# Kernel optimization log

Measured on AMD Instinct MI355X. Metric: run time of the kernel, lower is better.

Reference implementation:

```python
import jax, jax.numpy as jnp
import numpy as np

T, H, I, E, K = 1024, 1024, 1024, 16, 4
ALPHA, LIMIT, EPS = 1.702, 7.0, 1e-5


def setup_inputs() -> dict:
    key = jax.random.key(0)
    ks = jax.random.split(key, 8)
    return {
        "x": jax.random.normal(ks[0], (T, H), jnp.float32),
        "norm_w": jnp.ones((H,), jnp.float32) + 0.01 * jax.random.normal(ks[1], (H,), jnp.float32),
        "router_w": 0.02 * jax.random.normal(ks[2], (E, H), jnp.float32),
        "router_b": jnp.zeros((E,), jnp.float32),
        "w13": 0.02 * jax.random.normal(ks[3], (E, H, 2 * I), jnp.float32),
        "b13": 0.01 * jax.random.normal(ks[4], (E, 2 * I), jnp.float32),
        "w2": 0.02 * jax.random.normal(ks[5], (E, I, H), jnp.float32),
        "b2": 0.01 * jax.random.normal(ks[6], (E, H), jnp.float32),
        "manual_weights": jnp.zeros((1, E), jnp.float32),  # zeros => override branch inactive, as in __init__
        "layer_idx": 0,
    }


def _override(g, lw):
    # torch: log_softmax, then force pos-masked experts to max+0.01, neg-masked to min-0.01
    gl = jax.nn.log_softmax(g, axis=-1)
    mx = jnp.max(gl, axis=-1, keepdims=True)
    mn = jnp.min(gl, axis=-1, keepdims=True)
    gl = jnp.where((lw > 0)[None, :], mx + 0.01, gl)
    gl = jnp.where((lw < 0)[None, :], mn - 0.01, gl)
    return gl


def reference(x, norm_w, router_w, router_b, w13, b13, w2, b2, manual_weights, layer_idx):
    # RMSNorm (eps=1e-5)
    t = x * jax.lax.rsqrt(jnp.mean(x * x, axis=-1, keepdims=True) + EPS) * norm_w
    # router logits [T, E]
    g = t @ router_w.T + router_b
    # conditional manual logit override
    lw = manual_weights[layer_idx]
    g = jax.lax.cond(jnp.max(jnp.abs(lw)) > 0,
                     lambda gg: _override(gg, lw),
                     lambda gg: gg, g)
    # top-k routing, renormalize=True (softmax -> topk -> renorm)
    probs = jax.nn.softmax(g, axis=-1)
    topw, topi = jax.lax.top_k(probs, K)
    topw = topw / jnp.sum(topw, axis=-1, keepdims=True)
    # dense combine matrix [T, E] (sparse dispatch in the fused kernel)
    combine = jnp.zeros(g.shape, x.dtype).at[jnp.arange(g.shape[0])[:, None], topi].add(topw)
    # expert compute: gate_up GEMM + swigluoai + down GEMM (dense over experts for the reference)
    h = jnp.einsum('th,ehf->tef', t, w13) + b13          # [T, E, 2I]
    gate = jnp.minimum(h[..., :I], LIMIT)                # clamp(max=limit)
    up = jnp.clip(h[..., I:], -LIMIT, LIMIT)             # clamp(-limit, limit)
    act = (up + 1.0) * gate * jax.nn.sigmoid(ALPHA * gate)
    y = jnp.einsum('tei,eih->teh', act, w2) + b2         # [T, E, H]
    moe = jnp.einsum('te,teh->th', combine, y)           # weighted scatter-combine
    return x + moe
```

## Files before the change

### kernel.cpp

```cpp
#include <hip/hip_runtime.h>

#define T_    1024
#define H_    1024
#define IDIM  1024
#define E_    16
#define TOPK  4
#define ALPHA 1.702f
#define LIMIT 7.0f

typedef __bf16 bf16;
typedef __bf16 bf16x4 __attribute__((ext_vector_type(4)));
typedef __bf16 bf16x8 __attribute__((ext_vector_type(8)));
typedef float  f32x4  __attribute__((ext_vector_type(4)));

#define BARRIER() do { \
    asm volatile("s_waitcnt lgkmcnt(0)" ::: "memory"); \
    __builtin_amdgcn_s_barrier(); } while (0)

__global__ __launch_bounds__(256) void k_rms_router(
    const float* __restrict__ x, const float* __restrict__ nw,
    const float* __restrict__ rw, const float* __restrict__ rb,
    const float* __restrict__ mw, const int* __restrict__ lidx,
    bf16* __restrict__ tB, float* __restrict__ out,
    int* __restrict__ cnt, int* __restrict__ tok_list,
    float* __restrict__ wgt_list)
{
    const int t = blockIdx.x, tid = threadIdx.x;
    const int lane = tid & 63, wave = tid >> 6;
    __shared__ float tbuf[H_];
    __shared__ float red[4];
    __shared__ float logits[E_];

    float4 xv = ((const float4*)(x + (size_t)t * H_))[tid];
    float4 wv = ((const float4*)nw)[tid];
    float ssq = xv.x*xv.x + xv.y*xv.y + xv.z*xv.z + xv.w*xv.w;
    #pragma unroll
    for (int off = 32; off; off >>= 1) ssq += __shfl_xor(ssq, off);
    if (lane == 0) red[wave] = ssq;
    __syncthreads();
    const float rms = rsqrtf((red[0] + red[1] + red[2] + red[3]) * (1.0f / H_) + 1e-5f);

    float4 tv;
    tv.x = xv.x * rms * wv.x;
    tv.y = xv.y * rms * wv.y;
    tv.z = xv.z * rms * wv.z;
    tv.w = xv.w * rms * wv.w;

    ((float4*)(out + (size_t)t * H_))[tid] = xv;
    ((float4*)tbuf)[tid] = tv;
    bf16x4 tb = { (bf16)tv.x, (bf16)tv.y, (bf16)tv.z, (bf16)tv.w };
    *(bf16x4*)(tB + (size_t)t * H_ + tid * 4) = tb;
    __syncthreads();

    #pragma unroll
    for (int ei = 0; ei < 4; ++ei) {
        const int e = wave * 4 + ei;
        const float* wr = rw + (size_t)e * H_;
        float s = 0.f;
        #pragma unroll
        for (int j = 0; j < 16; ++j) {
            const int c = lane + j * 64;
            s += tbuf[c] * wr[c];
        }
        #pragma unroll
        for (int off = 32; off; off >>= 1) s += __shfl_xor(s, off);
        if (lane == 0) logits[e] = s + rb[e];
    }
    __syncthreads();

    if (tid == 0) {
        float g[E_];
        #pragma unroll
        for (int e = 0; e < E_; ++e) g[e] = logits[e];

        const int li = lidx[0];
        float ma = 0.f, lw[E_];
        #pragma unroll
        for (int e = 0; e < E_; ++e) { lw[e] = mw[li * E_ + e]; ma = fmaxf(ma, fabsf(lw[e])); }
        if (ma > 0.f) {
            float mx = -1e30f;
            for (int e = 0; e < E_; ++e) mx = fmaxf(mx, g[e]);
            float se = 0.f;
            for (int e = 0; e < E_; ++e) se += expf(g[e] - mx);
            const float lse = logf(se) + mx;
            float gl[E_], gmx = -1e30f, gmn = 1e30f;
            for (int e = 0; e < E_; ++e) { gl[e] = g[e] - lse; gmx = fmaxf(gmx, gl[e]); gmn = fminf(gmn, gl[e]); }
            for (int e = 0; e < E_; ++e) {
                if (lw[e] > 0.f)      gl[e] = gmx + 0.01f;
                else if (lw[e] < 0.f) gl[e] = gmn - 0.01f;
                g[e] = gl[e];
            }
        }

        float mx = -1e30f;
        #pragma unroll
        for (int e = 0; e < E_; ++e) mx = fmaxf(mx, g[e]);
        float p[E_];
        #pragma unroll
        for (int e = 0; e < E_; ++e) p[e] = expf(g[e] - mx);

        bool used[E_] = {};
        int   idx[TOPK];
        float twv[TOPK];
        float ssum = 0.f;
        for (int k = 0; k < TOPK; ++k) {
            int best = -1; float bv = -1e30f;
            for (int e = 0; e < E_; ++e)
                if (!used[e] && p[e] > bv) { bv = p[e]; best = e; }
            used[best] = true; idx[k] = best; twv[k] = bv; ssum += bv;
        }
        const float inv = 1.f / ssum;
        for (int k = 0; k < TOPK; ++k) {
            const int e = idx[k];
            const int slot = atomicAdd(&cnt[e], 1);
            tok_list[e * T_ + slot] = t;
            wgt_list[e * T_ + slot] = twv[k] * inv;
        }
    }
}

__global__ void k_scan(const int* __restrict__ cnt, int* __restrict__ base,
                       int* __restrict__ tiln, int* __restrict__ tile_e,
                       int* __restrict__ tile_m0)
{
    const int lane = threadIdx.x;
    int c = (lane < E_) ? cnt[lane] : 0;

    int s = c;
    #pragma unroll
    for (int off = 1; off < 16; off <<= 1) {
        int tv = __shfl_up(s, off);
        if ((lane & 15) >= off) s += tv;
    }
    if (lane < E_) base[lane] = s - c;
    if (lane == E_ - 1) base[E_] = s;

    int nt = (lane < E_) ? ((c + 63) >> 6) : 0;
    int ts = nt;
    #pragma unroll
    for (int off = 1; off < 16; off <<= 1) {
        int tv = __shfl_up(ts, off);
        if ((lane & 15) >= off) ts += tv;
    }
    if (lane == E_ - 1) tiln[0] = ts;
    if (lane < E_) {
        const int t0 = ts - nt;
        for (int i = 0; i < nt; ++i) {
            if (t0 + i < 96) { tile_e[t0 + i] = lane; tile_m0[t0 + i] = i * 64; }
        }
    }
}

__global__ __launch_bounds__(256) void k_repack(
    const float* __restrict__ W, bf16* __restrict__ out, int Ndim)
{
    __shared__ float tile[32][260];
    const int e = blockIdx.z, kb = blockIdx.y, n0 = blockIdx.x * 256;
    const int t = threadIdx.x;
    const int nbs = Ndim >> 4;

    const float* src = W + ((size_t)e * 1024 + (size_t)kb * 32) * Ndim + n0;
    #pragma unroll
    for (int i = 0; i < 8; ++i) {
        const int idx = i * 256 + t;
        const int k = idx >> 6, c4 = (idx & 63) * 4;
        float4 v = *(const float4*)(src + (size_t)k * Ndim + c4);
        *(float4*)&tile[k][c4] = v;
    }
    __syncthreads();

    const int f = t >> 4;
    const int lg = (t & 15) * 4;
    bf16* dst = out + (((size_t)(e * nbs + n0 / 16 + f)) * 32 + kb) * 512;
    #pragma unroll
    for (int li = 0; li < 4; ++li) {
        const int l = lg + li, q = l >> 4, r = l & 15;
        bf16x8 p;
        #pragma unroll
        for (int j = 0; j < 8; ++j) p[j] = (bf16)tile[q * 8 + j][f * 16 + r];
        *(bf16x8*)(dst + l * 8) = p;
    }
}

__global__ __launch_bounds__(256) void k_gateup3(
    const bf16* __restrict__ tB, const bf16* __restrict__ w13p,
    const float* __restrict__ b13, const int* __restrict__ cnt,
    const int* __restrict__ base, const int* __restrict__ tiln,
    const int* __restrict__ tile_e, const int* __restrict__ tile_m0,
    const int* __restrict__ tok_list, bf16* __restrict__ act)
{
    const int ti = blockIdx.y;
    if (ti >= tiln[0]) return;
    const int e  = tile_e[ti];
    const int m0 = tile_m0[ti];
    const int ne = cnt[e];

    const int tid = threadIdx.x, lane = tid & 63, wave = tid >> 6;
    const int q = lane >> 4, r = lane & 15;

    __shared__ __align__(16) bf16 As[8 * 64 * 8];

    const int m   = tid >> 2, kq = tid & 3;
    const int mf_s = m >> 4, r_s = m & 15;
    const int kc_s = kq >> 1, q_s = (kq & 1) * 2;
    bf16* wr0 = As + ((size_t)((mf_s * 2 + kc_s) * 64 + q_s * 16 + r_s)) * 8;
    bf16* wr1 = wr0 + 16 * 8;
    int srow = m0 + m; srow = srow < ne ? srow : ne - 1;
    const bf16* pA = tB + (size_t)tok_list[e * T_ + srow] * H_ + kq * 16;

    const int nb_g = blockIdx.x * 4 + wave;
    const bf16* pBg0 = w13p + ((size_t)(e * 128 + nb_g     ) * 32) * 512 + lane * 8;
    const bf16* pBu0 = w13p + ((size_t)(e * 128 + nb_g + 64) * 32) * 512 + lane * 8;

    f32x4 accg[4] = {};
    f32x4 accu[4] = {};
    uint4 ar0a, ar0b, ar1a, ar1b;
    bf16x8 bg0[2], bu0[2], bg1[2], bu1[2];

#define LOADA(A0, A1) do { \
    A0 = *(const uint4*)pA; A1 = *(const uint4*)(pA + 8); pA += 64; } while (0)
#define STAGEA(A0, A1) do { \
    *(uint4*)wr0 = A0; *(uint4*)wr1 = A1; } while (0)
#define LOADB(BG, BU, s) do { \
    const int ss_ = (s) < 16 ? (s) : 15; \
    BG[0] = *(const bf16x8*)(pBg0 + (size_t)ss_ * 1024); \
    BG[1] = *(const bf16x8*)(pBg0 + (size_t)ss_ * 1024 + 512); \
    BU[0] = *(const bf16x8*)(pBu0 + (size_t)ss_ * 1024); \
    BU[1] = *(const bf16x8*)(pBu0 + (size_t)ss_ * 1024 + 512); } while (0)
#define COMPUTE(BG, BU) do { \
    _Pragma("unroll") \
    for (int kc = 0; kc < 2; ++kc) { \
        bf16x8 afr[4]; \
        _Pragma("unroll") \
        for (int mf = 0; mf < 4; ++mf) \
            afr[mf] = *(const bf16x8*)(As + ((size_t)((mf * 2 + kc) * 64 + lane)) * 8); \
        _Pragma("unroll") \
        for (int mf = 0; mf < 4; ++mf) { \
            accg[mf] = __builtin_amdgcn_mfma_f32_16x16x32_bf16(afr[mf], BG[kc], accg[mf], 0, 0, 0); \
            accu[mf] = __builtin_amdgcn_mfma_f32_16x16x32_bf16(afr[mf], BU[kc], accu[mf], 0, 0, 0); \
        } \
    } } while (0)

    LOADA(ar0a, ar0b);
    LOADB(bg0, bu0, 0);
    LOADB(bg1, bu1, 1);
    #pragma unroll 1
    for (int kb = 0; kb < 16; kb += 2) {
        BARRIER();
        STAGEA(ar0a, ar0b);
        LOADA(ar1a, ar1b);
        BARRIER();
        COMPUTE(bg0, bu0);
        LOADB(bg0, bu0, kb + 2);

        BARRIER();
        STAGEA(ar1a, ar1b);
        LOADA(ar0a, ar0b);
        BARRIER();
        COMPUTE(bg1, bu1);
        LOADB(bg1, bu1, kb + 3);
    }
#undef LOADA
#undef STAGEA
#undef LOADB
#undef COMPUTE

    const int sb = base[e];
    const int cg = nb_g * 16 + r;
    const float bgv = b13[e * 2 * IDIM + cg];
    const float buv = b13[e * 2 * IDIM + IDIM + cg];
    #pragma unroll
    for (int mf = 0; mf < 4; ++mf) {
        #pragma unroll
        for (int rg = 0; rg < 4; ++rg) {
            const int row = mf * 16 + q * 4 + rg;
            if (m0 + row < ne) {
                const float hg = accg[mf][rg] + bgv;
                const float hu = accu[mf][rg] + buv;
                const float gt = fminf(hg, LIMIT);
                const float up = fminf(fmaxf(hu, -LIMIT), LIMIT);
                const float av = (up + 1.0f) * gt / (1.0f + expf(-ALPHA * gt));
                act[(size_t)(sb + m0 + row) * IDIM + cg] = (bf16)av;
            }
        }
    }
}

__global__ __launch_bounds__(256) void k_down3(
    const bf16* __restrict__ act, const bf16* __restrict__ w2p,
    const float* __restrict__ b2, const int* __restrict__ cnt,
    const int* __restrict__ base, const int* __restrict__ tiln,
    const int* __restrict__ tile_e, const int* __restrict__ tile_m0,
    const int* __restrict__ tok_list, const float* __restrict__ wgt_list,
    float* __restrict__ out)
{
    const int ti = blockIdx.y;
    if (ti >= tiln[0]) return;
    const int e  = tile_e[ti];
    const int m0 = tile_m0[ti];
    const int ne = cnt[e];
    const int sb = base[e];

    const int tid = threadIdx.x, lane = tid & 63, wave = tid >> 6;
    const int q = lane >> 4, r = lane & 15;

    __shared__ __align__(16) bf16 As[8 * 64 * 8];

    const int m   = tid >> 2, kq = tid & 3;
    const int mf_s = m >> 4, r_s = m & 15;
    const int kc_s = kq >> 1, q_s = (kq & 1) * 2;
    bf16* wr0 = As + ((size_t)((mf_s * 2 + kc_s) * 64 + q_s * 16 + r_s)) * 8;
    bf16* wr1 = wr0 + 16 * 8;
    int srow = m0 + m; srow = srow < ne ? srow : ne - 1;
    const bf16* pA = act + (size_t)(sb + srow) * IDIM + kq * 16;

    const int nb0 = blockIdx.x * 8 + wave * 2;
    const bf16* pB0b = w2p + ((size_t)(e * 64 + nb0    ) * 32) * 512 + lane * 8;
    const bf16* pB1b = w2p + ((size_t)(e * 64 + nb0 + 1) * 32) * 512 + lane * 8;

    f32x4 acc[4][2] = {};
    uint4 ar0a, ar0b, ar1a, ar1b;
    bf16x8 bA0[2], bB0[2], bA1[2], bB1[2];

#define LOADA(A0, A1) do { \
    A0 = *(const uint4*)pA; A1 = *(const uint4*)(pA + 8); pA += 64; } while (0)
#define STAGEA(A0, A1) do { \
    *(uint4*)wr0 = A0; *(uint4*)wr1 = A1; } while (0)
#define LOADB(B0, B1, s) do { \
    const int ss_ = (s) < 16 ? (s) : 15; \
    B0[0] = *(const bf16x8*)(pB0b + (size_t)ss_ * 1024); \
    B0[1] = *(const bf16x8*)(pB0b + (size_t)ss_ * 1024 + 512); \
    B1[0] = *(const bf16x8*)(pB1b + (size_t)ss_ * 1024); \
    B1[1] = *(const bf16x8*)(pB1b + (size_t)ss_ * 1024 + 512); } while (0)
#define COMPUTE(B0, B1) do { \
    _Pragma("unroll") \
    for (int kc = 0; kc < 2; ++kc) { \
        bf16x8 afr[4]; \
        _Pragma("unroll") \
        for (int mf = 0; mf < 4; ++mf) \
            afr[mf] = *(const bf16x8*)(As + ((size_t)((mf * 2 + kc) * 64 + lane)) * 8); \
        _Pragma("unroll") \
        for (int mf = 0; mf < 4; ++mf) { \
            acc[mf][0] = __builtin_amdgcn_mfma_f32_16x16x32_bf16(afr[mf], B0[kc], acc[mf][0], 0, 0, 0); \
            acc[mf][1] = __builtin_amdgcn_mfma_f32_16x16x32_bf16(afr[mf], B1[kc], acc[mf][1], 0, 0, 0); \
        } \
    } } while (0)

    LOADA(ar0a, ar0b);
    LOADB(bA0, bB0, 0);
    LOADB(bA1, bB1, 1);
    #pragma unroll 1
    for (int kb = 0; kb < 16; kb += 2) {
        BARRIER();
        STAGEA(ar0a, ar0b);
        LOADA(ar1a, ar1b);
        BARRIER();
        COMPUTE(bA0, bB0);
        LOADB(bA0, bB0, kb + 2);

        BARRIER();
        STAGEA(ar1a, ar1b);
        LOADA(ar0a, ar0b);
        BARRIER();
        COMPUTE(bA1, bB1);
        LOADB(bA1, bB1, kb + 3);
    }
#undef LOADA
#undef STAGEA
#undef LOADB
#undef COMPUTE

    #pragma unroll
    for (int nf = 0; nf < 2; ++nf) {
        const int ch = (nb0 + nf) * 16 + r;
        const float bb = b2[e * H_ + ch];
        #pragma unroll
        for (int mf = 0; mf < 4; ++mf) {
            #pragma unroll
            for (int rg = 0; rg < 4; ++rg) {
                const int row = mf * 16 + q * 4 + rg;
                const int s = m0 + row;
                if (s < ne) {
                    const int   tok = tok_list[e * T_ + s];
                    const float w   = wgt_list[e * T_ + s];
                    atomicAdd(&out[(size_t)tok * H_ + ch], w * (acc[mf][nf][rg] + bb));
                }
            }
        }
    }
}

__global__ __launch_bounds__(256) void k_gateup(
    const bf16* __restrict__ tB, const float* __restrict__ w13,
    const float* __restrict__ b13, const int* __restrict__ cnt,
    const int* __restrict__ base, const int* __restrict__ tok_list,
    bf16* __restrict__ act)
{
    const int e  = blockIdx.z;
    const int ne = cnt[e];
    const int m0 = blockIdx.y * 64;
    if (m0 >= ne) return;
    const int n0  = blockIdx.x * 64;
    const int tid = threadIdx.x, lane = tid & 63, wave = tid >> 6;

    __shared__ __align__(16) bf16 As[64][40];
    __shared__ __align__(16) bf16 Bg[64][40];
    __shared__ __align__(16) bf16 Bu[64][40];
    __shared__ int stok[64];

    if (tid < 64) {
        const int s = m0 + tid;
        stok[tid] = (s < ne) ? tok_list[e * T_ + s] : -1;
    }
    __syncthreads();

    const int ar = tid >> 2, ak = (tid & 3) * 8;
    const int atok = stok[ar];
    const int bn = tid & 63, bk = wave * 8;
    const size_t wrow = (size_t)(2 * IDIM);
    const float* wbase = w13 + (size_t)e * H_ * wrow + n0 + bn;

    const int wm = wave >> 1, wn = wave & 1;
    const int q = lane >> 4, r = lane & 15;
    f32x4 accg[2][2] = {};
    f32x4 accu[2][2] = {};

    for (int kb = 0; kb < H_ / 32; ++kb) {
        __syncthreads();
        uint4 av = make_uint4(0u, 0u, 0u, 0u);
        if (atok >= 0)
            av = *(const uint4*)(tB + (size_t)atok * H_ + kb * 32 + ak);
        *(uint4*)&As[ar][ak] = av;
        {
            const float* src = wbase + (size_t)(kb * 32 + bk) * wrow;
            bf16x8 pg, pu;
            #pragma unroll
            for (int j = 0; j < 8; ++j) {
                pg[j] = (bf16)src[(size_t)j * wrow];
                pu[j] = (bf16)src[(size_t)j * wrow + IDIM];
            }
            *(bf16x8*)&Bg[bn][bk] = pg;
            *(bf16x8*)&Bu[bn][bk] = pu;
        }
        __syncthreads();
        bf16x8 a[2], bg[2], bu[2];
        a[0]  = *(const bf16x8*)&As[wm * 32 +      r][q * 8];
        a[1]  = *(const bf16x8*)&As[wm * 32 + 16 + r][q * 8];
        bg[0] = *(const bf16x8*)&Bg[wn * 32 +      r][q * 8];
        bg[1] = *(const bf16x8*)&Bg[wn * 32 + 16 + r][q * 8];
        bu[0] = *(const bf16x8*)&Bu[wn * 32 +      r][q * 8];
        bu[1] = *(const bf16x8*)&Bu[wn * 32 + 16 + r][q * 8];
        #pragma unroll
        for (int im = 0; im < 2; ++im)
            #pragma unroll
            for (int in = 0; in < 2; ++in) {
                accg[im][in] = __builtin_amdgcn_mfma_f32_16x16x32_bf16(a[im], bg[in], accg[im][in], 0, 0, 0);
                accu[im][in] = __builtin_amdgcn_mfma_f32_16x16x32_bf16(a[im], bu[in], accu[im][in], 0, 0, 0);
            }
    }

    const int sb = base[e];
    #pragma unroll
    for (int im = 0; im < 2; ++im)
        #pragma unroll
        for (int in = 0; in < 2; ++in)
            #pragma unroll
            for (int rg = 0; rg < 4; ++rg) {
                const int row = wm * 32 + im * 16 + q * 4 + rg;
                const int col = wn * 32 + in * 16 + r;
                if (m0 + row < ne) {
                    const float hg = accg[im][in][rg] + b13[e * 2 * IDIM + n0 + col];
                    const float hu = accu[im][in][rg] + b13[e * 2 * IDIM + IDIM + n0 + col];
                    const float gt = fminf(hg, LIMIT);
                    const float up = fminf(fmaxf(hu, -LIMIT), LIMIT);
                    const float av = (up + 1.0f) * gt / (1.0f + expf(-ALPHA * gt));
                    act[(size_t)(sb + m0 + row) * IDIM + n0 + col] = (bf16)av;
                }
            }
}

__global__ __launch_bounds__(256) void k_down(
    const bf16* __restrict__ act, const float* __restrict__ w2,
    const float* __restrict__ b2, const int* __restrict__ cnt,
    const int* __restrict__ base, const int* __restrict__ tok_list,
    const float* __restrict__ wgt_list, float* __restrict__ out)
{
    const int e  = blockIdx.z;
    const int ne = cnt[e];
    const int m0 = blockIdx.y * 64;
    if (m0 >= ne) return;
    const int n0  = blockIdx.x * 64;
    const int tid = threadIdx.x, lane = tid & 63, wave = tid >> 6;

    __shared__ __align__(16) bf16 As[64][40];
    __shared__ __align__(16) bf16 Bs[64][40];
    __shared__ int   stok[64];
    __shared__ float swgt[64];

    if (tid < 64) {
        const int s = m0 + tid;
        stok[tid] = (s < ne) ? tok_list[e * T_ + s] : -1;
        swgt[tid] = (s < ne) ? wgt_list[e * T_ + s] : 0.f;
    }
    __syncthreads();

    const int sb = base[e];
    const int ar = tid >> 2, ak = (tid & 3) * 8;
    const bool arow_ok = (m0 + ar) < ne;
    const int bn = tid & 63, bk = wave * 8;
    const float* wbase = w2 + (size_t)e * IDIM * H_ + n0 + bn;

    const int wm = wave >> 1, wn = wave & 1;
    const int q = lane >> 4, r = lane & 15;
    f32x4 acc[2][2] = {};

    for (int kb = 0; kb < IDIM / 32; ++kb) {
        __syncthreads();
        uint4 av = make_uint4(0u, 0u, 0u, 0u);
        if (arow_ok)
            av = *(const uint4*)(act + (size_t)(sb + m0 + ar) * IDIM + kb * 32 + ak);
        *(uint4*)&As[ar][ak] = av;
        {
            const float* src = wbase + (size_t)(kb * 32 + bk) * H_;
            bf16x8 pb;
            #pragma unroll
            for (int j = 0; j < 8; ++j) pb[j] = (bf16)src[(size_t)j * H_];
            *(bf16x8*)&Bs[bn][bk] = pb;
        }
        __syncthreads();
        bf16x8 a[2], b[2];
        a[0] = *(const bf16x8*)&As[wm * 32 +      r][q * 8];
        a[1] = *(const bf16x8*)&As[wm * 32 + 16 + r][q * 8];
        b[0] = *(const bf16x8*)&Bs[wn * 32 +      r][q * 8];
        b[1] = *(const bf16x8*)&Bs[wn * 32 + 16 + r][q * 8];
        #pragma unroll
        for (int im = 0; im < 2; ++im)
            #pragma unroll
            for (int in = 0; in < 2; ++in)
                acc[im][in] = __builtin_amdgcn_mfma_f32_16x16x32_bf16(a[im], b[in], acc[im][in], 0, 0, 0);
    }

    #pragma unroll
    for (int im = 0; im < 2; ++im)
        #pragma unroll
        for (int in = 0; in < 2; ++in)
            #pragma unroll
            for (int rg = 0; rg < 4; ++rg) {
                const int row = wm * 32 + im * 16 + q * 4 + rg;
                const int col = wn * 32 + in * 16 + r;
                if (m0 + row < ne) {
                    const int   tok = stok[row];
                    const float w   = swgt[row];
                    atomicAdd(&out[(size_t)tok * H_ + n0 + col], w * (acc[im][in][rg] + b2[e * H_ + n0 + col]));
                }
            }
}

extern "C" void kernel_launch(void* const* d_in, const int* in_sizes, int n_in,
                              void* d_out, int out_size, void* d_ws, size_t ws_size,
                              hipStream_t stream)
{
    const float* x        = (const float*)d_in[0];
    const float* norm_w   = (const float*)d_in[1];
    const float* router_w = (const float*)d_in[2];
    const float* router_b = (const float*)d_in[3];
    const float* w13      = (const float*)d_in[4];
    const float* b13      = (const float*)d_in[5];
    const float* w2       = (const float*)d_in[6];
    const float* b2       = (const float*)d_in[7];
    const float* manual_w = (const float*)d_in[8];
    const int*   layer_i  = (const int*)d_in[9];
    float* out = (float*)d_out;

    char* ws = (char*)d_ws;
    bf16*  tB   = (bf16*)ws;
    bf16*  act  = (bf16*)(ws + (2ull << 20));
    char*  meta = ws + (10ull << 20);
    int*   cnt      = (int*)meta;
    int*   basep    = (int*)(meta + 64);
    int*   tiln     = (int*)(meta + 256);
    int*   tile_e   = (int*)(meta + 512);
    int*   tile_m0  = (int*)(meta + 1024);
    int*   tok_list = (int*)(meta + (16ull << 10));
    float* wgt_list = (float*)(meta + (16ull << 10) + (64ull << 10));
    bf16*  w13p     = (bf16*)(ws + (12ull << 20));
    bf16*  w2p      = (bf16*)(ws + (76ull << 20));

    const bool fast = ws_size >= (108ull << 20);

    hipMemsetAsync(cnt, 0, E_ * sizeof(int), stream);

    k_rms_router<<<T_, 256, 0, stream>>>(x, norm_w, router_w, router_b,
                                         manual_w, layer_i, tB, out,
                                         cnt, tok_list, wgt_list);
    k_scan<<<1, 64, 0, stream>>>(cnt, basep, tiln, tile_e, tile_m0);

    if (fast) {
        dim3 gr13(2 * IDIM / 256, 32, E_);
        k_repack<<<gr13, 256, 0, stream>>>(w13, w13p, 2 * IDIM);
        dim3 gr2(H_ / 256, 32, E_);
        k_repack<<<gr2, 256, 0, stream>>>(w2, w2p, H_);

        dim3 gg(16, 80);
        k_gateup3<<<gg, 256, 0, stream>>>(tB, w13p, b13, cnt, basep, tiln,
                                          tile_e, tile_m0, tok_list, act);
        dim3 gd(8, 80);
        k_down3<<<gd, 256, 0, stream>>>(act, w2p, b2, cnt, basep, tiln,
                                        tile_e, tile_m0, tok_list, wgt_list, out);
    } else {
        dim3 gg(IDIM / 64, T_ / 64, E_);
        k_gateup<<<gg, 256, 0, stream>>>(tB, w13, b13, cnt, basep, tok_list, act);
        dim3 gd(H_ / 64, T_ / 64, E_);
        k_down<<<gd, 256, 0, stream>>>(act, w2, b2, cnt, basep, tok_list, wgt_list, out);
    }
}
```

Baseline: 401.7 us.

## Fuse weight fp32-to-bf16 conversion into GEMM tiles and inline routing scan

Drops the separate repack kernels that converted all expert weights to packed bf16 each call. The GEMM kernels now load fp32 weight rows directly, convert them in registers and stage them into a padded shared-memory B tile. The single-block scan kernel is also removed, and each block computes its own expert/tile assignment from the counts. The aim is to avoid writing and re-reading a full bf16 weight copy and to cut two launches, at the cost of more LDS traffic, more register pressure and fp32 global reads in the main loop.

```diff
diff --git a/kernel.cpp b/kernel.cpp
--- a/kernel.cpp
+++ b/kernel.cpp
@@ -119,86 +119,44 @@
     }
 }
 
-__global__ void k_scan(const int* __restrict__ cnt, int* __restrict__ base,
-                       int* __restrict__ tiln, int* __restrict__ tile_e,
-                       int* __restrict__ tile_m0)
+__device__ __forceinline__ void inline_scan(const int* __restrict__ cnt,
+                                            int ti, int tid, int* sm)
 {
-    const int lane = threadIdx.x;
-    int c = (lane < E_) ? cnt[lane] : 0;
-
-    int s = c;
-    #pragma unroll
-    for (int off = 1; off < 16; off <<= 1) {
-        int tv = __shfl_up(s, off);
-        if ((lane & 15) >= off) s += tv;
-    }
-    if (lane < E_) base[lane] = s - c;
-    if (lane == E_ - 1) base[E_] = s;
-
-    int nt = (lane < E_) ? ((c + 63) >> 6) : 0;
-    int ts = nt;
-    #pragma unroll
-    for (int off = 1; off < 16; off <<= 1) {
-        int tv = __shfl_up(ts, off);
-        if ((lane & 15) >= off) ts += tv;
-    }
-    if (lane == E_ - 1) tiln[0] = ts;
-    if (lane < E_) {
-        const int t0 = ts - nt;
-        for (int i = 0; i < nt; ++i) {
-            if (t0 + i < 96) { tile_e[t0 + i] = lane; tile_m0[t0 + i] = i * 64; }
-        }
-    }
+    if (tid == 0) {
+        int c0[E_];
+        #pragma unroll
+        for (int e = 0; e < E_; ++e) c0[e] = cnt[e];
+        int s = 0, nt = 0, ee = 0, mm0 = 0, nee = 0, sbb = 0;
+        #pragma unroll
+        for (int e = 0; e < E_; ++e) {
+            const int c = c0[e];
+            const int tcnt = (c + 63) >> 6;
+            if (ti >= nt && ti < nt + tcnt) {
+                ee = e; mm0 = (ti - nt) * 64; nee = c; sbb = s;
+            }
+            s += c; nt += tcnt;
+        }
+        sm[0] = nt; sm[1] = ee; sm[2] = mm0; sm[3] = nee; sm[4] = sbb;
+    }
+    __syncthreads();
 }
 
-__global__ __launch_bounds__(256) void k_repack(
-    const float* __restrict__ W, bf16* __restrict__ out, int Ndim)
-{
-    __shared__ float tile[32][260];
-    const int e = blockIdx.z, kb = blockIdx.y, n0 = blockIdx.x * 256;
-    const int t = threadIdx.x;
-    const int nbs = Ndim >> 4;
-
-    const float* src = W + ((size_t)e * 1024 + (size_t)kb * 32) * Ndim + n0;
-    #pragma unroll
-    for (int i = 0; i < 8; ++i) {
-        const int idx = i * 256 + t;
-        const int k = idx >> 6, c4 = (idx & 63) * 4;
-        float4 v = *(const float4*)(src + (size_t)k * Ndim + c4);
-        *(float4*)&tile[k][c4] = v;
-    }
-    __syncthreads();
-
-    const int f = t >> 4;
-    const int lg = (t & 15) * 4;
-    bf16* dst = out + (((size_t)(e * nbs + n0 / 16 + f)) * 32 + kb) * 512;
-    #pragma unroll
-    for (int li = 0; li < 4; ++li) {
-        const int l = lg + li, q = l >> 4, r = l & 15;
-        bf16x8 p;
-        #pragma unroll
-        for (int j = 0; j < 8; ++j) p[j] = (bf16)tile[q * 8 + j][f * 16 + r];
-        *(bf16x8*)(dst + l * 8) = p;
-    }
-}
-
-__global__ __launch_bounds__(256) void k_gateup3(
-    const bf16* __restrict__ tB, const bf16* __restrict__ w13p,
+__global__ __launch_bounds__(256) void k_gateup7(
+    const bf16* __restrict__ tB, const float* __restrict__ w13,
     const float* __restrict__ b13, const int* __restrict__ cnt,
-    const int* __restrict__ base, const int* __restrict__ tiln,
-    const int* __restrict__ tile_e, const int* __restrict__ tile_m0,
     const int* __restrict__ tok_list, bf16* __restrict__ act)
 {
-    const int ti = blockIdx.y;
-    if (ti >= tiln[0]) return;
-    const int e  = tile_e[ti];
-    const int m0 = tile_m0[ti];
-    const int ne = cnt[e];
-
+    const int ti = blockIdx.y, bx = blockIdx.x;
     const int tid = threadIdx.x, lane = tid & 63, wave = tid >> 6;
     const int q = lane >> 4, r = lane & 15;
 
     __shared__ __align__(16) bf16 As[8 * 64 * 8];
+    __shared__ __align__(16) bf16 Bs[1032 * 8];
+    __shared__ int sm[5];
+
+    inline_scan(cnt, ti, tid, sm);
+    if (ti >= sm[0]) return;
+    const int e = sm[1], m0 = sm[2], ne = sm[3], sb = sm[4];
 
     const int m   = tid >> 2, kq = tid & 3;
     const int mf_s = m >> 4, r_s = m & 15;
@@ -208,64 +166,77 @@
     int srow = m0 + m; srow = srow < ne ? srow : ne - 1;
     const bf16* pA = tB + (size_t)tok_list[e * T_ + srow] * H_ + kq * 16;
 
-    const int nb_g = blockIdx.x * 4 + wave;
-    const bf16* pBg0 = w13p + ((size_t)(e * 128 + nb_g     ) * 32) * 512 + lane * 8;
-    const bf16* pBu0 = w13p + ((size_t)(e * 128 + nb_g + 64) * 32) * 512 + lane * 8;
+    const int c4 = tid & 31, q6 = tid >> 5;
+    const int kcs = q6 >> 2, qs = q6 & 3;
+    const int cc = c4 * 4;
+    const int fB = c4 >> 2, r0 = (c4 & 3) * 4;
+    const int RB = fB * 2 + kcs;
+    bf16* bwr = Bs + ((size_t)(RB * 64 + (RB >> 1) + qs * 16 + r0)) * 8;
+    const int col = (cc < 64) ? (bx * 64 + cc) : (IDIM + bx * 64 + (cc - 64));
+    const float* pB = w13 + (size_t)e * H_ * (2 * IDIM)
+                          + (size_t)(kcs * 32 + qs * 8) * (2 * IDIM) + col;
 
     f32x4 accg[4] = {};
     f32x4 accu[4] = {};
-    uint4 ar0a, ar0b, ar1a, ar1b;
-    bf16x8 bg0[2], bu0[2], bg1[2], bu1[2];
-
-#define LOADA(A0, A1) do { \
-    A0 = *(const uint4*)pA; A1 = *(const uint4*)(pA + 8); pA += 64; } while (0)
-#define STAGEA(A0, A1) do { \
-    *(uint4*)wr0 = A0; *(uint4*)wr1 = A1; } while (0)
-#define LOADB(BG, BU, s) do { \
-    const int ss_ = (s) < 16 ? (s) : 15; \
-    BG[0] = *(const bf16x8*)(pBg0 + (size_t)ss_ * 1024); \
-    BG[1] = *(const bf16x8*)(pBg0 + (size_t)ss_ * 1024 + 512); \
-    BU[0] = *(const bf16x8*)(pBu0 + (size_t)ss_ * 1024); \
-    BU[1] = *(const bf16x8*)(pBu0 + (size_t)ss_ * 1024 + 512); } while (0)
-#define COMPUTE(BG, BU) do { \
+    uint4  a0a, a0b, a1a, a1b;
+    f32x4  br0[8], br1[8];
+
+#define LOADA(A0, A1, s) do { const int ss_ = (s) < 16 ? (s) : 15; \
+    A0 = *(const uint4*)(pA + ss_ * 64); \
+    A1 = *(const uint4*)(pA + ss_ * 64 + 8); } while (0)
+#define LOADB(BR, s) do { const int ss_ = (s) < 16 ? (s) : 15; \
+    _Pragma("unroll") \
+    for (int j = 0; j < 8; ++j) \
+        BR[j] = *(const f32x4*)(pB + (size_t)(ss_ * 64 + j) * (2 * IDIM)); } while (0)
+#define STAGEA(A0, A1) do { *(uint4*)wr0 = A0; *(uint4*)wr1 = A1; } while (0)
+#define STAGEB(BR) do { \
+    _Pragma("unroll") \
+    for (int rr = 0; rr < 4; ++rr) { \
+        bf16x8 p; \
+        _Pragma("unroll") \
+        for (int j = 0; j < 8; ++j) p[j] = (bf16)BR[j][rr]; \
+        *(bf16x8*)(bwr + rr * 8) = p; \
+    } } while (0)
+#define COMPUTE() do { \
     _Pragma("unroll") \
     for (int kc = 0; kc < 2; ++kc) { \
         bf16x8 afr[4]; \
         _Pragma("unroll") \
         for (int mf = 0; mf < 4; ++mf) \
             afr[mf] = *(const bf16x8*)(As + ((size_t)((mf * 2 + kc) * 64 + lane)) * 8); \
+        const int Rg = wave * 2 + kc, Ru = (wave + 4) * 2 + kc; \
+        bf16x8 bg = *(const bf16x8*)(Bs + ((size_t)(Rg * 64 + (Rg >> 1) + lane)) * 8); \
+        bf16x8 bu = *(const bf16x8*)(Bs + ((size_t)(Ru * 64 + (Ru >> 1) + lane)) * 8); \
         _Pragma("unroll") \
         for (int mf = 0; mf < 4; ++mf) { \
-            accg[mf] = __builtin_amdgcn_mfma_f32_16x16x32_bf16(afr[mf], BG[kc], accg[mf], 0, 0, 0); \
-            accu[mf] = __builtin_amdgcn_mfma_f32_16x16x32_bf16(afr[mf], BU[kc], accu[mf], 0, 0, 0); \
+            accg[mf] = __builtin_amdgcn_mfma_f32_16x16x32_bf16(afr[mf], bg, accg[mf], 0, 0, 0); \
+            accu[mf] = __builtin_amdgcn_mfma_f32_16x16x32_bf16(afr[mf], bu, accu[mf], 0, 0, 0); \
         } \
     } } while (0)
 
-    LOADA(ar0a, ar0b);
-    LOADB(bg0, bu0, 0);
-    LOADB(bg1, bu1, 1);
+    LOADA(a0a, a0b, 0);
+    LOADB(br0, 0);
     #pragma unroll 1
     for (int kb = 0; kb < 16; kb += 2) {
         BARRIER();
-        STAGEA(ar0a, ar0b);
-        LOADA(ar1a, ar1b);
-        BARRIER();
-        COMPUTE(bg0, bu0);
-        LOADB(bg0, bu0, kb + 2);
-
-        BARRIER();
-        STAGEA(ar1a, ar1b);
-        LOADA(ar0a, ar0b);
-        BARRIER();
-        COMPUTE(bg1, bu1);
-        LOADB(bg1, bu1, kb + 3);
+        STAGEA(a0a, a0b);  STAGEB(br0);
+        LOADA(a1a, a1b, kb + 1);  LOADB(br1, kb + 1);
+        BARRIER();
+        COMPUTE();
+
+        BARRIER();
+        STAGEA(a1a, a1b);  STAGEB(br1);
+        LOADA(a0a, a0b, kb + 2);  LOADB(br0, kb + 2);
+        BARRIER();
+        COMPUTE();
     }
 #undef LOADA
+#undef LOADB
 #undef STAGEA
-#undef LOADB
+#undef STAGEB
 #undef COMPUTE
 
-    const int sb = base[e];
+    const int nb_g = bx * 4 + wave;
     const int cg = nb_g * 16 + r;
     const float bgv = b13[e * 2 * IDIM + cg];
     const float buv = b13[e * 2 * IDIM + IDIM + cg];
@@ -286,25 +257,23 @@
     }
 }
 
-__global__ __launch_bounds__(256) void k_down3(
-    const bf16* __restrict__ act, const bf16* __restrict__ w2p,
+__global__ __launch_bounds__(256) void k_down7(
+    const bf16* __restrict__ act, const float* __restrict__ w2,
     const float* __restrict__ b2, const int* __restrict__ cnt,
-    const int* __restrict__ base, const int* __restrict__ tiln,
-    const int* __restrict__ tile_e, const int* __restrict__ tile_m0,
     const int* __restrict__ tok_list, const float* __restrict__ wgt_list,
     float* __restrict__ out)
 {
-    const int ti = blockIdx.y;
-    if (ti >= tiln[0]) return;
-    const int e  = tile_e[ti];
-    const int m0 = tile_m0[ti];
-    const int ne = cnt[e];
-    const int sb = base[e];
-
+    const int ti = blockIdx.y, bx = blockIdx.x;
     const int tid = threadIdx.x, lane = tid & 63, wave = tid >> 6;
     const int q = lane >> 4, r = lane & 15;
 
     __shared__ __align__(16) bf16 As[8 * 64 * 8];
+    __shared__ __align__(16) bf16 Bs[1032 * 8];
+    __shared__ int sm[5];
+
+    inline_scan(cnt, ti, tid, sm);
+    if (ti >= sm[0]) return;
+    const int e = sm[1], m0 = sm[2], ne = sm[3], sb = sm[4];
 
     const int m   = tid >> 2, kq = tid & 3;
     const int mf_s = m >> 4, r_s = m & 15;
@@ -314,62 +283,75 @@
     int srow = m0 + m; srow = srow < ne ? srow : ne - 1;
     const bf16* pA = act + (size_t)(sb + srow) * IDIM + kq * 16;
 
-    const int nb0 = blockIdx.x * 8 + wave * 2;
-    const bf16* pB0b = w2p + ((size_t)(e * 64 + nb0    ) * 32) * 512 + lane * 8;
-    const bf16* pB1b = w2p + ((size_t)(e * 64 + nb0 + 1) * 32) * 512 + lane * 8;
+    const int c4 = tid & 31, q6 = tid >> 5;
+    const int kcs = q6 >> 2, qs = q6 & 3;
+    const int cc = c4 * 4;
+    const int fB = c4 >> 2, r0 = (c4 & 3) * 4;
+    const int RB = fB * 2 + kcs;
+    bf16* bwr = Bs + ((size_t)(RB * 64 + (RB >> 1) + qs * 16 + r0)) * 8;
+    const float* pB = w2 + (size_t)e * IDIM * H_
+                         + (size_t)(kcs * 32 + qs * 8) * H_ + bx * 128 + cc;
 
     f32x4 acc[4][2] = {};
-    uint4 ar0a, ar0b, ar1a, ar1b;
-    bf16x8 bA0[2], bB0[2], bA1[2], bB1[2];
-
-#define LOADA(A0, A1) do { \
-    A0 = *(const uint4*)pA; A1 = *(const uint4*)(pA + 8); pA += 64; } while (0)
-#define STAGEA(A0, A1) do { \
-    *(uint4*)wr0 = A0; *(uint4*)wr1 = A1; } while (0)
-#define LOADB(B0, B1, s) do { \
-    const int ss_ = (s) < 16 ? (s) : 15; \
-    B0[0] = *(const bf16x8*)(pB0b + (size_t)ss_ * 1024); \
-    B0[1] = *(const bf16x8*)(pB0b + (size_t)ss_ * 1024 + 512); \
-    B1[0] = *(const bf16x8*)(pB1b + (size_t)ss_ * 1024); \
-    B1[1] = *(const bf16x8*)(pB1b + (size_t)ss_ * 1024 + 512); } while (0)
-#define COMPUTE(B0, B1) do { \
+    uint4  a0a, a0b, a1a, a1b;
+    f32x4  br0[8], br1[8];
+
+#define LOADA(A0, A1, s) do { const int ss_ = (s) < 16 ? (s) : 15; \
+    A0 = *(const uint4*)(pA + ss_ * 64); \
+    A1 = *(const uint4*)(pA + ss_ * 64 + 8); } while (0)
+#define LOADB(BR, s) do { const int ss_ = (s) < 16 ? (s) : 15; \
+    _Pragma("unroll") \
+    for (int j = 0; j < 8; ++j) \
+        BR[j] = *(const f32x4*)(pB + (size_t)(ss_ * 64 + j) * H_); } while (0)
+#define STAGEA(A0, A1) do { *(uint4*)wr0 = A0; *(uint4*)wr1 = A1; } while (0)
+#define STAGEB(BR) do { \
+    _Pragma("unroll") \
+    for (int rr = 0; rr < 4; ++rr) { \
+        bf16x8 p; \
+        _Pragma("unroll") \
+        for (int j = 0; j < 8; ++j) p[j] = (bf16)BR[j][rr]; \
+        *(bf16x8*)(bwr + rr * 8) = p; \
+    } } while (0)
+#define COMPUTE() do { \
     _Pragma("unroll") \
     for (int kc = 0; kc < 2; ++kc) { \
         bf16x8 afr[4]; \
         _Pragma("unroll") \
         for (int mf = 0; mf < 4; ++mf) \
             afr[mf] = *(const bf16x8*)(As + ((size_t)((mf * 2 + kc) * 64 + lane)) * 8); \
+        const int R0 = (wave * 2) * 2 + kc, R1 = (wave * 2 + 1) * 2 + kc; \
+        bf16x8 b0 = *(const bf16x8*)(Bs + ((size_t)(R0 * 64 + (R0 >> 1) + lane)) * 8); \
+        bf16x8 b1 = *(const bf16x8*)(Bs + ((size_t)(R1 * 64 + (R1 >> 1) + lane)) * 8); \
         _Pragma("unroll") \
         for (int mf = 0; mf < 4; ++mf) { \
-            acc[mf][0] = __builtin_amdgcn_mfma_f32_16x16x32_bf16(afr[mf], B0[kc], acc[mf][0], 0, 0, 0); \
-            acc[mf][1] = __builtin_amdgcn_mfma_f32_16x16x32_bf16(afr[mf], B1[kc], acc[mf][1], 0, 0, 0); \
+            acc[mf][0] = __builtin_amdgcn_mfma_f32_16x16x32_bf16(afr[mf], b0, acc[mf][0], 0, 0, 0); \
+            acc[mf][1] = __builtin_amdgcn_mfma_f32_16x16x32_bf16(afr[mf], b1, acc[mf][1], 0, 0, 0); \
         } \
     } } while (0)
 
-    LOADA(ar0a, ar0b);
-    LOADB(bA0, bB0, 0);
-    LOADB(bA1, bB1, 1);
+    LOADA(a0a, a0b, 0);
+    LOADB(br0, 0);
     #pragma unroll 1
     for (int kb = 0; kb < 16; kb += 2) {
         BARRIER();
-        STAGEA(ar0a, ar0b);
-        LOADA(ar1a, ar1b);
-        BARRIER();
-        COMPUTE(bA0, bB0);
-        LOADB(bA0, bB0, kb + 2);
-
-        BARRIER();
-        STAGEA(ar1a, ar1b);
-        LOADA(ar0a, ar0b);
-        BARRIER();
-        COMPUTE(bA1, bB1);
-        LOADB(bA1, bB1, kb + 3);
+        STAGEA(a0a, a0b);  STAGEB(br0);
+        LOADA(a1a, a1b, kb + 1);  LOADB(br1, kb + 1);
+        BARRIER();
+        COMPUTE();
+
+        BARRIER();
+        STAGEA(a1a, a1b);  STAGEB(br1);
+        LOADA(a0a, a0b, kb + 2);  LOADB(br0, kb + 2);
+        BARRIER();
+        COMPUTE();
     }
 #undef LOADA
+#undef LOADB
 #undef STAGEA
-#undef LOADB
+#undef STAGEB
 #undef COMPUTE
 
+    const int nb0 = bx * 8 + wave * 2;
     #pragma unroll
     for (int nf = 0; nf < 2; ++nf) {
         const int ch = (nb0 + nf) * 16 + r;
@@ -388,172 +370,6 @@
             }
         }
     }
-}
-
-__global__ __launch_bounds__(256) void k_gateup(
-    const bf16* __restrict__ tB, const float* __restrict__ w13,
-    const float* __restrict__ b13, const int* __restrict__ cnt,
-    const int* __restrict__ base, const int* __restrict__ tok_list,
-    bf16* __restrict__ act)
-{
-    const int e  = blockIdx.z;
-    const int ne = cnt[e];
-    const int m0 = blockIdx.y * 64;
-    if (m0 >= ne) return;
-    const int n0  = blockIdx.x * 64;
-    const int tid = threadIdx.x, lane = tid & 63, wave = tid >> 6;
-
-    __shared__ __align__(16) bf16 As[64][40];
-    __shared__ __align__(16) bf16 Bg[64][40];
-    __shared__ __align__(16) bf16 Bu[64][40];
-    __shared__ int stok[64];
-
-    if (tid < 64) {
-        const int s = m0 + tid;
-        stok[tid] = (s < ne) ? tok_list[e * T_ + s] : -1;
-    }
-    __syncthreads();
-
-    const int ar = tid >> 2, ak = (tid & 3) * 8;
-    const int atok = stok[ar];
-    const int bn = tid & 63, bk = wave * 8;
-    const size_t wrow = (size_t)(2 * IDIM);
-    const float* wbase = w13 + (size_t)e * H_ * wrow + n0 + bn;
-
-    const int wm = wave >> 1, wn = wave & 1;
-    const int q = lane >> 4, r = lane & 15;
-    f32x4 accg[2][2] = {};
-    f32x4 accu[2][2] = {};
-
-    for (int kb = 0; kb < H_ / 32; ++kb) {
-        __syncthreads();
-        uint4 av = make_uint4(0u, 0u, 0u, 0u);
-        if (atok >= 0)
-            av = *(const uint4*)(tB + (size_t)atok * H_ + kb * 32 + ak);
-        *(uint4*)&As[ar][ak] = av;
-        {
-            const float* src = wbase + (size_t)(kb * 32 + bk) * wrow;
-            bf16x8 pg, pu;
-            #pragma unroll
-            for (int j = 0; j < 8; ++j) {
-                pg[j] = (bf16)src[(size_t)j * wrow];
-                pu[j] = (bf16)src[(size_t)j * wrow + IDIM];
-            }
-            *(bf16x8*)&Bg[bn][bk] = pg;
-            *(bf16x8*)&Bu[bn][bk] = pu;
-        }
-        __syncthreads();
-        bf16x8 a[2], bg[2], bu[2];
-        a[0]  = *(const bf16x8*)&As[wm * 32 +      r][q * 8];
-        a[1]  = *(const bf16x8*)&As[wm * 32 + 16 + r][q * 8];
-        bg[0] = *(const bf16x8*)&Bg[wn * 32 +      r][q * 8];
-        bg[1] = *(const bf16x8*)&Bg[wn * 32 + 16 + r][q * 8];
-        bu[0] = *(const bf16x8*)&Bu[wn * 32 +      r][q * 8];
-        bu[1] = *(const bf16x8*)&Bu[wn * 32 + 16 + r][q * 8];
-        #pragma unroll
-        for (int im = 0; im < 2; ++im)
-            #pragma unroll
-            for (int in = 0; in < 2; ++in) {
-                accg[im][in] = __builtin_amdgcn_mfma_f32_16x16x32_bf16(a[im], bg[in], accg[im][in], 0, 0, 0);
-                accu[im][in] = __builtin_amdgcn_mfma_f32_16x16x32_bf16(a[im], bu[in], accu[im][in], 0, 0, 0);
-            }
-    }
-
-    const int sb = base[e];
-    #pragma unroll
-    for (int im = 0; im < 2; ++im)
-        #pragma unroll
-        for (int in = 0; in < 2; ++in)
-            #pragma unroll
-            for (int rg = 0; rg < 4; ++rg) {
-                const int row = wm * 32 + im * 16 + q * 4 + rg;
-                const int col = wn * 32 + in * 16 + r;
-                if (m0 + row < ne) {
-                    const float hg = accg[im][in][rg] + b13[e * 2 * IDIM + n0 + col];
-                    const float hu = accu[im][in][rg] + b13[e * 2 * IDIM + IDIM + n0 + col];
-                    const float gt = fminf(hg, LIMIT);
-                    const float up = fminf(fmaxf(hu, -LIMIT), LIMIT);
-                    const float av = (up + 1.0f) * gt / (1.0f + expf(-ALPHA * gt));
-                    act[(size_t)(sb + m0 + row) * IDIM + n0 + col] = (bf16)av;
-                }
-            }
-}
-
-__global__ __launch_bounds__(256) void k_down(
-    const bf16* __restrict__ act, const float* __restrict__ w2,
-    const float* __restrict__ b2, const int* __restrict__ cnt,
-    const int* __restrict__ base, const int* __restrict__ tok_list,
-    const float* __restrict__ wgt_list, float* __restrict__ out)
-{
-    const int e  = blockIdx.z;
-    const int ne = cnt[e];
-    const int m0 = blockIdx.y * 64;
-    if (m0 >= ne) return;
-    const int n0  = blockIdx.x * 64;
-    const int tid = threadIdx.x, lane = tid & 63, wave = tid >> 6;
-
-    __shared__ __align__(16) bf16 As[64][40];
-    __shared__ __align__(16) bf16 Bs[64][40];
-    __shared__ int   stok[64];
-    __shared__ float swgt[64];
-
-    if (tid < 64) {
-        const int s = m0 + tid;
-        stok[tid] = (s < ne) ? tok_list[e * T_ + s] : -1;
-        swgt[tid] = (s < ne) ? wgt_list[e * T_ + s] : 0.f;
-    }
-    __syncthreads();
-
-    const int sb = base[e];
-    const int ar = tid >> 2, ak = (tid & 3) * 8;
-    const bool arow_ok = (m0 + ar) < ne;
-    const int bn = tid & 63, bk = wave * 8;
-    const float* wbase = w2 + (size_t)e * IDIM * H_ + n0 + bn;
-
-    const int wm = wave >> 1, wn = wave & 1;
-    const int q = lane >> 4, r = lane & 15;
-    f32x4 acc[2][2] = {};
-
-    for (int kb = 0; kb < IDIM / 32; ++kb) {
-        __syncthreads();
-        uint4 av = make_uint4(0u, 0u, 0u, 0u);
-        if (arow_ok)
-            av = *(const uint4*)(act + (size_t)(sb + m0 + ar) * IDIM + kb * 32 + ak);
-        *(uint4*)&As[ar][ak] = av;
-        {
-            const float* src = wbase + (size_t)(kb * 32 + bk) * H_;
-            bf16x8 pb;
-            #pragma unroll
-            for (int j = 0; j < 8; ++j) pb[j] = (bf16)src[(size_t)j * H_];
-            *(bf16x8*)&Bs[bn][bk] = pb;
-        }
-        __syncthreads();
-        bf16x8 a[2], b[2];
-        a[0] = *(const bf16x8*)&As[wm * 32 +      r][q * 8];
-        a[1] = *(const bf16x8*)&As[wm * 32 + 16 + r][q * 8];
-        b[0] = *(const bf16x8*)&Bs[wn * 32 +      r][q * 8];
-        b[1] = *(const bf16x8*)&Bs[wn * 32 + 16 + r][q * 8];
-        #pragma unroll
-        for (int im = 0; im < 2; ++im)
-            #pragma unroll
-            for (int in = 0; in < 2; ++in)
-                acc[im][in] = __builtin_amdgcn_mfma_f32_16x16x32_bf16(a[im], b[in], acc[im][in], 0, 0, 0);
-    }
-
-    #pragma unroll
-    for (int im = 0; im < 2; ++im)
-        #pragma unroll
-        for (int in = 0; in < 2; ++in)
-            #pragma unroll
-            for (int rg = 0; rg < 4; ++rg) {
-                const int row = wm * 32 + im * 16 + q * 4 + rg;
-                const int col = wn * 32 + in * 16 + r;
-                if (m0 + row < ne) {
-                    const int   tok = stok[row];
-                    const float w   = swgt[row];
-                    atomicAdd(&out[(size_t)tok * H_ + n0 + col], w * (acc[im][in][rg] + b2[e * H_ + n0 + col]));
-                }
-            }
 }
 
 extern "C" void kernel_launch(void* const* d_in, const int* in_sizes, int n_in,
@@ -577,40 +393,17 @@
     bf16*  act  = (bf16*)(ws + (2ull << 20));
     char*  meta = ws + (10ull << 20);
     int*   cnt      = (int*)meta;
-    int*   basep    = (int*)(meta + 64);
-    int*   tiln     = (int*)(meta + 256);
-    int*   tile_e   = (int*)(meta + 512);
-    int*   tile_m0  = (int*)(meta + 1024);
     int*   tok_list = (int*)(meta + (16ull << 10));
     float* wgt_list = (float*)(meta + (16ull << 10) + (64ull << 10));
-    bf16*  w13p     = (bf16*)(ws + (12ull << 20));
-    bf16*  w2p      = (bf16*)(ws + (76ull << 20));
-
-    const bool fast = ws_size >= (108ull << 20);
 
     hipMemsetAsync(cnt, 0, E_ * sizeof(int), stream);
 
     k_rms_router<<<T_, 256, 0, stream>>>(x, norm_w, router_w, router_b,
                                          manual_w, layer_i, tB, out,
                                          cnt, tok_list, wgt_list);
-    k_scan<<<1, 64, 0, stream>>>(cnt, basep, tiln, tile_e, tile_m0);
-
-    if (fast) {
-        dim3 gr13(2 * IDIM / 256, 32, E_);
-        k_repack<<<gr13, 256, 0, stream>>>(w13, w13p, 2 * IDIM);
-        dim3 gr2(H_ / 256, 32, E_);
-        k_repack<<<gr2, 256, 0, stream>>>(w2, w2p, H_);
-
-        dim3 gg(16, 80);
-        k_gateup3<<<gg, 256, 0, stream>>>(tB, w13p, b13, cnt, basep, tiln,
-                                          tile_e, tile_m0, tok_list, act);
-        dim3 gd(8, 80);
-        k_down3<<<gd, 256, 0, stream>>>(act, w2p, b2, cnt, basep, tiln,
-                                        tile_e, tile_m0, tok_list, wgt_list, out);
-    } else {
-        dim3 gg(IDIM / 64, T_ / 64, E_);
-        k_gateup<<<gg, 256, 0, stream>>>(tB, w13, b13, cnt, basep, tok_list, act);
-        dim3 gd(H_ / 64, T_ / 64, E_);
-        k_down<<<gd, 256, 0, stream>>>(act, w2, b2, cnt, basep, tok_list, wgt_list, out);
-    }
+
+    dim3 gg(16, 80);
+    k_gateup7<<<gg, 256, 0, stream>>>(tB, w13, b13, cnt, tok_list, act);
+    dim3 gd(8, 80);
+    k_down7<<<gd, 256, 0, stream>>>(act, w2, b2, cnt, tok_list, wgt_list, out);
 }
```

Result: faster. 373.2 us (-7.1%).
